# Kernel optimization log

Measured on AMD Instinct MI355X. Metric: run time of the kernel, lower is better.

## Reference

```python
import jax, jax.numpy as jnp
import numpy as np

B, T, F = 8, 4096, 256

def setup_inputs() -> dict:
    key = jax.random.key(0)
    ks = jax.random.split(key, 10)
    s = 1.0 / np.sqrt(F)
    return {
        "x": jax.random.normal(ks[0], (B, T, F), dtype=jnp.float32),
        "Wq_w": jax.random.normal(ks[1], (F, F), dtype=jnp.float32) * s,
        "Wq_b": jax.random.normal(ks[2], (F,), dtype=jnp.float32) * 0.01,
        "Wk_w": jax.random.normal(ks[3], (F, F), dtype=jnp.float32) * s,
        "Wk_b": jax.random.normal(ks[4], (F,), dtype=jnp.float32) * 0.01,
        "Wv_w": jax.random.normal(ks[5], (F, F), dtype=jnp.float32) * s,
        "Wv_b": jax.random.normal(ks[6], (F,), dtype=jnp.float32) * 0.01,
        "w": jax.random.normal(ks[7], (T, T), dtype=jnp.float32) * 0.02,
        "out_w": jax.random.normal(ks[8], (F, F), dtype=jnp.float32) * s,
        "out_b": jax.random.normal(ks[9], (F,), dtype=jnp.float32) * 0.01,
    }

def reference(x, Wq_w, Wq_b, Wk_w, Wk_b, Wv_w, Wv_b, w, out_w, out_b):
    # Linear layers (torch convention: y = x @ W.T + b)
    Q = x @ Wq_w.T + Wq_b                      # [B, T, F]
    K = x @ Wk_w.T + Wk_b                      # [B, T, F]
    V = x @ Wv_w.T + Wv_b                      # [B, T, F]
    Q_sig = jax.nn.sigmoid(Q)
    # Stabilized exponentials (faithful: w over rows, K over FEATURE dim)
    exp_w = jnp.exp(w - jnp.max(w, axis=-1, keepdims=True))        # [T, T]
    exp_K = jnp.exp(K - jnp.max(K, axis=-1, keepdims=True))        # [B, T, F]
    num = jnp.einsum('ts,bsf->btf', exp_w, exp_K * V)              # [B, T, F]
    den = jnp.einsum('ts,bsf->btf', exp_w, exp_K)                  # [B, T, F]
    Yt = Q_sig * (num / den)
    return Yt @ out_w.T + out_b
```

## Files before the change

### kernel.cpp

```cpp
#include <hip/hip_runtime.h>
#include <hip/hip_bf16.h>

#define BB 8
#define TT 4096
#define FF 256
#define BT 32768

typedef unsigned short u16;
typedef __attribute__((ext_vector_type(8))) short short8;
typedef __attribute__((ext_vector_type(4))) float f32x4;
typedef __attribute__((ext_vector_type(4))) unsigned int u32x4;

static __device__ __forceinline__ float bf2f(u16 u) {
    union { unsigned int i; float f; } v; v.i = ((unsigned int)u) << 16; return v.f;
}
static __device__ __forceinline__ u16 f2bf(float f) {
    union { float f; unsigned int i; } v; v.f = f;
    unsigned int x = v.i;
    return (u16)((x + 0x7fffu + ((x >> 16) & 1u)) >> 16);
}

typedef const __attribute__((address_space(1))) void gvoid_t;
typedef __attribute__((address_space(3))) void svoid_t;

__global__ __launch_bounds__(256) void expw_kernel(const float* __restrict__ w,
                                                   u16* __restrict__ ew) {
    __shared__ float red[256];
    int row = blockIdx.x;
    int tid = threadIdx.x;
    const float* wr = w + (size_t)row * TT;

    f32x4 vals[4];
    float m = -1e30f;
#pragma unroll
    for (int v = 0; v < 4; ++v) {
        int idx = (v * 256 + tid) * 4;
        vals[v] = *(const f32x4*)(wr + idx);
#pragma unroll
        for (int j = 0; j < 4; ++j) m = fmaxf(m, vals[v][j]);
    }
    red[tid] = m;
    __syncthreads();
    for (int s = 128; s > 0; s >>= 1) {
        if (tid < s) red[tid] = fmaxf(red[tid], red[tid + s]);
        __syncthreads();
    }
    float rm = red[0];
#pragma unroll
    for (int v = 0; v < 4; ++v) {
        int idx = (v * 256 + tid) * 4;
        float e0 = expf(vals[v][0] - rm), e1 = expf(vals[v][1] - rm);
        float e2 = expf(vals[v][2] - rm), e3 = expf(vals[v][3] - rm);
        uint2 pk;
        pk.x = (unsigned int)f2bf(e0) | ((unsigned int)f2bf(e1) << 16);
        pk.y = (unsigned int)f2bf(e2) | ((unsigned int)f2bf(e3) << 16);
        *(uint2*)(ew + (size_t)row * TT + idx) = pk;
    }
}

__global__ __launch_bounds__(256) void cvt_bf16_kernel(const float* __restrict__ in,
                                                       u16* __restrict__ out, int n4) {
    int i = blockIdx.x * 256 + threadIdx.x;
    if (i < n4) {
        f32x4 v = ((const f32x4*)in)[i];
        uint2 pk;
        pk.x = (unsigned int)f2bf(v[0]) | ((unsigned int)f2bf(v[1]) << 16);
        pk.y = (unsigned int)f2bf(v[2]) | ((unsigned int)f2bf(v[3]) << 16);
        ((uint2*)out)[i] = pk;
    }
}

__global__ __launch_bounds__(256) void cvt_weights_kernel(const float* __restrict__ wq,
                                                          const float* __restrict__ wo,
                                                          const float* __restrict__ wk,
                                                          const float* __restrict__ wv,
                                                          u16* __restrict__ wqb,
                                                          u16* __restrict__ wob,
                                                          u16* __restrict__ wkv) {
    int i = blockIdx.x * 256 + threadIdx.x;
    int which = i >> 14, j = i & 16383;
    int idx = j * 4;
    if (which == 0) {
        f32x4 v = *(const f32x4*)(wq + idx);
        uint2 pk;
        pk.x = (unsigned int)f2bf(v[0]) | ((unsigned int)f2bf(v[1]) << 16);
        pk.y = (unsigned int)f2bf(v[2]) | ((unsigned int)f2bf(v[3]) << 16);
        *(uint2*)(wqb + idx) = pk;
    } else if (which == 1) {
        f32x4 v = *(const f32x4*)(wo + idx);
        uint2 pk;
        pk.x = (unsigned int)f2bf(v[0]) | ((unsigned int)f2bf(v[1]) << 16);
        pk.y = (unsigned int)f2bf(v[2]) | ((unsigned int)f2bf(v[3]) << 16);
        *(uint2*)(wob + idx) = pk;
    } else {
        int f = idx >> 8, c = idx & 255;
        f32x4 a = *(const f32x4*)(wk + idx);
        f32x4 b = *(const f32x4*)(wv + idx);
        uint2 pa, pb;
        pa.x = (unsigned int)f2bf(a[0]) | ((unsigned int)f2bf(a[1]) << 16);
        pa.y = (unsigned int)f2bf(a[2]) | ((unsigned int)f2bf(a[3]) << 16);
        pb.x = (unsigned int)f2bf(b[0]) | ((unsigned int)f2bf(b[1]) << 16);
        pb.y = (unsigned int)f2bf(b[2]) | ((unsigned int)f2bf(b[3]) << 16);
        *(uint2*)(wkv + (size_t)(2 * f) * 256 + c) = pa;
        *(uint2*)(wkv + (size_t)(2 * f + 1) * 256 + c) = pb;
    }
}

template <int MODE>
__global__ __launch_bounds__(256) void gemm_nt(const u16* __restrict__ A,
                                               const u16* __restrict__ Bm,
                                               const float* __restrict__ bias,
                                               void* __restrict__ Call,
                                               int M, int N, int K) {
    __shared__ u16 As[128 * 32];
    __shared__ u16 Bs[128 * 32];

    int tid = threadIdx.x;
    int lane = tid & 63;
    int w = tid >> 6;
    int wr = w >> 1, wc = w & 1;
    int fr = lane & 15, kg = lane >> 4;

    f32x4 acc[4][4];
#pragma unroll
    for (int m = 0; m < 4; ++m)
#pragma unroll
        for (int n = 0; n < 4; ++n) acc[m][n] = (f32x4){0.f, 0.f, 0.f, 0.f};

    int bm = blockIdx.x, bn = blockIdx.y;
    int nk = K >> 5;

    int srow = tid >> 2;
    int schunk = (tid & 3) << 3;
    const u16* aBase = A + (size_t)(bm * 128 + srow) * K + schunk;
    const u16* bBase = Bm + (size_t)(bn * 128 + srow) * K + schunk;
    size_t half = (size_t)64 * K;

    for (int kt = 0; kt < nk; ++kt) {
        __syncthreads();
        int ko = kt << 5;
        __builtin_amdgcn_global_load_lds((gvoid_t*)(aBase + ko), (svoid_t*)&As[tid * 8], 16, 0, 0);
        __builtin_amdgcn_global_load_lds((gvoid_t*)(aBase + half + ko), (svoid_t*)&As[2048 + tid * 8], 16, 0, 0);
        __builtin_amdgcn_global_load_lds((gvoid_t*)(bBase + ko), (svoid_t*)&Bs[tid * 8], 16, 0, 0);
        __builtin_amdgcn_global_load_lds((gvoid_t*)(bBase + half + ko), (svoid_t*)&Bs[2048 + tid * 8], 16, 0, 0);
        __syncthreads();

        short8 af[4], bfr[4];
#pragma unroll
        for (int m = 0; m < 4; ++m)
            af[m] = *(const short8*)&As[(wr * 64 + m * 16 + fr) * 32 + kg * 8];
#pragma unroll
        for (int n = 0; n < 4; ++n)
            bfr[n] = *(const short8*)&Bs[(wc * 64 + n * 16 + fr) * 32 + kg * 8];
#pragma unroll
        for (int m = 0; m < 4; ++m)
#pragma unroll
            for (int n = 0; n < 4; ++n)
                acc[m][n] = __builtin_amdgcn_mfma_f32_16x16x32_bf16(af[m], bfr[n], acc[m][n], 0, 0, 0);
    }

    int row0 = bm * 128 + wr * 64;
    int col0 = bn * 128 + wc * 64;
#pragma unroll
    for (int n = 0; n < 4; ++n) {
        int col = col0 + n * 16 + fr;
        float bv = bias ? bias[col] : 0.0f;
#pragma unroll
        for (int m = 0; m < 4; ++m) {
            int rbase = row0 + m * 16 + kg * 4;
#pragma unroll
            for (int i = 0; i < 4; ++i) {
                float val = acc[m][n][i] + bv;
                size_t idx = (size_t)(rbase + i) * N + col;
                if (MODE == 0)
                    ((float*)Call)[idx] = val;
                else if (MODE == 1)
                    ((u16*)Call)[idx] = f2bf(1.0f / (1.0f + expf(-val)));
                else
                    ((u16*)Call)[idx] = f2bf(val);
            }
        }
    }
}

__global__ __launch_bounds__(512) void kv_mt_kernel(const u16* __restrict__ xbf,
                                                    const u16* __restrict__ wkv,
                                                    const float* __restrict__ bk,
                                                    const float* __restrict__ bv,
                                                    u16* __restrict__ mt) {
    __shared__ u16 As[128 * 32];
    __shared__ u16 Bs[512 * 32];
    __shared__ float rmax4[128][4];

    int tid = threadIdx.x;
    int lane = tid & 63, wid = tid >> 6;
    int fr = lane & 15, kg = lane >> 4;
    int wr = wid >> 2, wc = wid & 3;
    int row0g = blockIdx.x * 128;

    f32x4 acc[4][8];
#pragma unroll
    for (int m = 0; m < 4; ++m)
#pragma unroll
        for (int n = 0; n < 8; ++n) acc[m][n] = (f32x4){0.f, 0.f, 0.f, 0.f};

    const u16* aSrc = xbf + (size_t)(row0g + (tid >> 2)) * 256 + (tid & 3) * 8;
    const u16* bSrc = wkv + (size_t)(tid >> 2) * 256 + (tid & 3) * 8;

    for (int ks = 0; ks < 8; ++ks) {
        __syncthreads();
        __builtin_amdgcn_global_load_lds((gvoid_t*)(aSrc + ks * 32), (svoid_t*)&As[tid * 8], 16, 0, 0);
#pragma unroll
        for (int c = 0; c < 4; ++c)
            __builtin_amdgcn_global_load_lds((gvoid_t*)(bSrc + (size_t)c * 128 * 256 + ks * 32),
                                             (svoid_t*)&Bs[c * 4096 + tid * 8], 16, 0, 0);
        __syncthreads();

        short8 af[4], bfr[8];
#pragma unroll
        for (int m = 0; m < 4; ++m)
            af[m] = *(const short8*)&As[(wr * 64 + m * 16 + fr) * 32 + kg * 8];
#pragma unroll
        for (int n = 0; n < 8; ++n)
            bfr[n] = *(const short8*)&Bs[(wc * 128 + n * 16 + fr) * 32 + kg * 8];
#pragma unroll
        for (int m = 0; m < 4; ++m)
#pragma unroll
            for (int n = 0; n < 8; ++n)
                acc[m][n] = __builtin_amdgcn_mfma_f32_16x16x32_bf16(af[m], bfr[n], acc[m][n], 0, 0, 0);
    }

    int par = fr & 1;
#pragma unroll
    for (int n = 0; n < 8; ++n) {
        int col = wc * 128 + n * 16 + fr;
        int f = col >> 1;
        float bvv = par ? bv[f] : bk[f];
#pragma unroll
        for (int m = 0; m < 4; ++m)
#pragma unroll
            for (int i = 0; i < 4; ++i) acc[m][n][i] += bvv;
    }

    float rmax[4][4];
#pragma unroll
    for (int m = 0; m < 4; ++m)
#pragma unroll
        for (int i = 0; i < 4; ++i) {
            float mx = -1e30f;
#pragma unroll
            for (int n = 0; n < 8; ++n) mx = fmaxf(mx, par ? -1e30f : acc[m][n][i]);
            mx = fmaxf(mx, __shfl_xor(mx, 2));
            mx = fmaxf(mx, __shfl_xor(mx, 4));
            mx = fmaxf(mx, __shfl_xor(mx, 8));
            mx = fmaxf(mx, __shfl_xor(mx, 1));
            rmax[m][i] = mx;
        }
    if (fr == 0) {
#pragma unroll
        for (int m = 0; m < 4; ++m)
#pragma unroll
            for (int i = 0; i < 4; ++i)
                rmax4[wr * 64 + m * 16 + kg * 4 + i][wc] = rmax[m][i];
    }
    __syncthreads();
#pragma unroll
    for (int m = 0; m < 4; ++m)
#pragma unroll
        for (int i = 0; i < 4; ++i) {
            f32x4 r4 = *(const f32x4*)rmax4[wr * 64 + m * 16 + kg * 4 + i];
            rmax[m][i] = fmaxf(fmaxf(r4[0], r4[1]), fmaxf(r4[2], r4[3]));
        }

    int b = row0g >> 12;
    int tcb = (row0g & 4095) + wr * 64;
#pragma unroll
    for (int n = 0; n < 8; ++n) {
        int col = wc * 128 + n * 16 + fr;
        int f = col >> 1;
        size_t rowmt = (size_t)(b * 512 + 2 * f + (par ? 0 : 1));
#pragma unroll
        for (int m = 0; m < 4; ++m) {
            int tc = tcb + m * 16 + kg * 4;
            u16 o[4];
#pragma unroll
            for (int i = 0; i < 4; ++i) {
                float v = acc[m][n][i];
                float ek = expf(v - rmax[m][i]);
                float ekx = __shfl_xor(ek, 1);
                float outv = par ? (ekx * v) : ek;
                o[i] = f2bf(outv);
            }
            uint2 pk;
            pk.x = (unsigned int)o[0] | ((unsigned int)o[1] << 16);
            pk.y = (unsigned int)o[2] | ((unsigned int)o[3] << 16);
            *(uint2*)(mt + rowmt * TT + tc) = pk;
        }
    }
}

#define GLDS(src, eoff) \
    __builtin_amdgcn_global_load_lds((gvoid_t*)(src), (svoid_t*)&L[eoff], 16, 0, 0)

#define STAGE8(P_, KS_) do {                                                   \
    _Pragma("unroll")                                                          \
    for (int i_ = 0; i_ < 4; ++i_) {                                           \
        GLDS(sA + (size_t)i_ * 64 * 4096 + (KS_) * 64,                         \
             (P_) * 16384 + i_ * 4096 + dst);                                  \
        GLDS(sB + (size_t)i_ * 64 * 4096 + (KS_) * 64,                         \
             32768 + (P_) * 16384 + i_ * 4096 + dst);                          \
    }                                                                          \
} while (0)

__global__ __launch_bounds__(512, 2) void gemm256_nt(const u16* __restrict__ A,
                                                     const u16* __restrict__ B,
                                                     const u16* __restrict__ qsig,
                                                     u16* __restrict__ yt) {
    __shared__ u16 L[65536];
    const int K = 4096;
    int tid = threadIdx.x;
    int lane = tid & 63, wid = tid >> 6;
    int fr = lane & 15, kg = lane >> 4;
    int wr = wid >> 2, wc = wid & 3;

    int bid = blockIdx.x;
    int xcd = bid & 7;
    int sl = bid >> 3;
    int bm = (xcd & 3) * 4 + (sl >> 3);
    int bn = (xcd >> 2) * 8 + (sl & 7);

    const char* LB = (const char*)L;

    int x0 = (kg * 16) ^ ((fr & 7) << 4);
    int x1 = (64 + kg * 16) ^ ((fr & 7) << 4);
    int arow = (wr * 128 + fr) * 128;
    int brow = (wc * 64 + fr) * 128;

    int scol = ((tid & 7) * 8) ^ (((tid >> 3) & 7) << 3);
    const u16* sA = A + (size_t)(bm * 256 + (tid >> 3)) * K + scol;
    const u16* sB = B + (size_t)(bn * 256 + (tid >> 3)) * K + scol;
    int dst = tid * 8;

    f32x4 acc[8][4];
#pragma unroll
    for (int m = 0; m < 8; ++m)
#pragma unroll
        for (int n = 0; n < 4; ++n) acc[m][n] = (f32x4){0.f, 0.f, 0.f, 0.f};

    STAGE8(0, 0);
    asm volatile("s_waitcnt vmcnt(0)" ::: "memory");
    __builtin_amdgcn_sched_barrier(0);
    __builtin_amdgcn_s_barrier();

#pragma unroll 1
    for (int t = 0; t < 64; ++t) {
        int p = t & 1;
        const char* abase = LB + p * 32768;
        const char* bbase = LB + 65536 + p * 32768;

        int ks = (t + 1 < 64) ? t + 1 : 0;
        STAGE8(p ^ 1, ks);

        short8 bfr[4][2], af[4][2];
#pragma unroll
        for (int nf = 0; nf < 4; ++nf) {
            const char* rb = bbase + brow + nf * 2048;
            bfr[nf][0] = *(const short8*)(rb + x0);
            bfr[nf][1] = *(const short8*)(rb + x1);
        }
#pragma unroll
        for (int mf = 0; mf < 4; ++mf) {
            const char* rb = abase + arow + mf * 2048;
            af[mf][0] = *(const short8*)(rb + x0);
            af[mf][1] = *(const short8*)(rb + x1);
        }
        asm volatile("s_waitcnt lgkmcnt(0)" ::: "memory");
        __builtin_amdgcn_sched_barrier(0);
        __builtin_amdgcn_s_setprio(1);
#pragma unroll
        for (int mf = 0; mf < 4; ++mf)
#pragma unroll
            for (int nf = 0; nf < 4; ++nf) {
                acc[mf][nf] = __builtin_amdgcn_mfma_f32_16x16x32_bf16(af[mf][0], bfr[nf][0], acc[mf][nf], 0, 0, 0);
                acc[mf][nf] = __builtin_amdgcn_mfma_f32_16x16x32_bf16(af[mf][1], bfr[nf][1], acc[mf][nf], 0, 0, 0);
            }
        __builtin_amdgcn_s_setprio(0);
#pragma unroll
        for (int mf = 0; mf < 4; ++mf) {
            const char* rb = abase + arow + (mf + 4) * 2048;
            af[mf][0] = *(const short8*)(rb + x0);
            af[mf][1] = *(const short8*)(rb + x1);
        }
        asm volatile("s_waitcnt lgkmcnt(0)" ::: "memory");
        __builtin_amdgcn_sched_barrier(0);
        __builtin_amdgcn_s_setprio(1);
#pragma unroll
        for (int mf = 0; mf < 4; ++mf)
#pragma unroll
            for (int nf = 0; nf < 4; ++nf) {
                acc[mf + 4][nf] = __builtin_amdgcn_mfma_f32_16x16x32_bf16(af[mf][0], bfr[nf][0], acc[mf + 4][nf], 0, 0, 0);
                acc[mf + 4][nf] = __builtin_amdgcn_mfma_f32_16x16x32_bf16(af[mf][1], bfr[nf][1], acc[mf + 4][nf], 0, 0, 0);
            }
        __builtin_amdgcn_s_setprio(0);
        asm volatile("s_waitcnt vmcnt(0)" ::: "memory");
        __builtin_amdgcn_sched_barrier(0);
        __builtin_amdgcn_s_barrier();
    }

    int colgb = bn * 256 + wc * 64;
    int row0 = bm * 256 + wr * 128;
    int par = fr & 1;
#pragma unroll
    for (int n = 0; n < 4; ++n) {
        int colg = colgb + n * 16 + fr;
        int b = colg >> 9;
        int f = (colg & 511) >> 1;
#pragma unroll
        for (int m = 0; m < 8; ++m) {
            int tr0 = row0 + m * 16 + kg * 4;
            float v0 = acc[m][n][0], v1 = acc[m][n][1];
            float v2 = acc[m][n][2], v3 = acc[m][n][3];
            float o0 = __shfl_xor(v0, 1), o1 = __shfl_xor(v1, 1);
            float o2 = __shfl_xor(v2, 1), o3 = __shfl_xor(v3, 1);
            float nA = par ? o2 : v0, dA = par ? v2 : o0;
            float nB = par ? o3 : v1, dB = par ? v3 : o1;
            int iA = par ? 2 : 0;
            size_t idxA = ((size_t)(b * 4096 + tr0 + iA) << 8) + f;
            size_t idxB = idxA + 256;
            float qA = bf2f(qsig[idxA]);
            float qB = bf2f(qsig[idxB]);
            yt[idxA] = f2bf(qA * nA * __builtin_amdgcn_rcpf(dA));
            yt[idxB] = f2bf(qB * nB * __builtin_amdgcn_rcpf(dB));
        }
    }
}

extern "C" void kernel_launch(void* const* d_in, const int* in_sizes, int n_in,
                              void* d_out, int out_size, void* d_ws, size_t ws_size,
                              hipStream_t stream) {
    const float* x  = (const float*)d_in[0];
    const float* wq = (const float*)d_in[1];
    const float* bq = (const float*)d_in[2];
    const float* wk = (const float*)d_in[3];
    const float* bk = (const float*)d_in[4];
    const float* wv = (const float*)d_in[5];
    const float* bv = (const float*)d_in[6];
    const float* w  = (const float*)d_in[7];
    const float* wo = (const float*)d_in[8];
    const float* bo = (const float*)d_in[9];

    char* p = (char*)d_ws;
    u16* expw = (u16*)p; p += (size_t)TT * TT * 2;
    u16* xbf  = (u16*)p; p += (size_t)BT * FF * 2;
    u16* wqb  = (u16*)p; p += (size_t)FF * FF * 2;
    u16* wob  = (u16*)p; p += (size_t)FF * FF * 2;
    u16* wkv  = (u16*)p; p += (size_t)2 * FF * FF * 2;
    u16* qsig = (u16*)p; p += (size_t)BT * FF * 2;
    u16* mt   = (u16*)p; p += (size_t)BB * 512 * TT * 2;
    u16* yt = xbf;

    expw_kernel<<<TT, 256, 0, stream>>>(w, expw);

    cvt_bf16_kernel<<<(BT * FF / 4 + 255) / 256, 256, 0, stream>>>(x, xbf, BT * FF / 4);
    cvt_weights_kernel<<<192, 256, 0, stream>>>(wq, wo, wk, wv, wqb, wob, wkv);

    dim3 gp(BT / 128, FF / 128, 1);
    gemm_nt<1><<<gp, 256, 0, stream>>>(xbf, wqb, bq, qsig, BT, FF, FF);

    kv_mt_kernel<<<BT / 128, 512, 0, stream>>>(xbf, wkv, bk, bv, mt);

    gemm256_nt<<<256, 512, 0, stream>>>(expw, mt, qsig, yt);

    gemm_nt<0><<<gp, 256, 0, stream>>>(yt, wob, bo, (float*)d_out, BT, FF, FF);
}
```

Measured before the change: 191.7 us.

## Split GEMM main loop into four phases interleaving staging, LDS reads and MFMA

Splits each k-step of the 256x256 GEMM into four phases, each handling one half of the A or B tile and one k-half of the fragments. Every phase issues a quarter of the next-tile global-to-LDS loads, then its LDS fragment reads, then its MFMAs, with extra workgroup barriers between phases. The aim is to spread memory issue across the compute so loads and MFMA overlap better, and to hold fewer fragment registers (4+4 short8 instead of 8+8). The cost is three more s_barriers per iteration and shorter MFMA bursts, which could leave more time waiting at barriers.

```diff
diff --git a/kernel.cpp b/kernel.cpp
--- a/kernel.cpp
+++ b/kernel.cpp
@@ -302,14 +302,19 @@
 #define GLDS(src, eoff) \
     __builtin_amdgcn_global_load_lds((gvoid_t*)(src), (svoid_t*)&L[eoff], 16, 0, 0)
 
-#define STAGE8(P_, KS_) do {                                                   \
+#define STAGE_H(SRC, RO, P_, H_, KS_) do {                                     \
     _Pragma("unroll")                                                          \
-    for (int i_ = 0; i_ < 4; ++i_) {                                           \
-        GLDS(sA + (size_t)i_ * 64 * 4096 + (KS_) * 64,                         \
-             (P_) * 16384 + i_ * 4096 + dst);                                  \
-        GLDS(sB + (size_t)i_ * 64 * 4096 + (KS_) * 64,                         \
-             32768 + (P_) * 16384 + i_ * 4096 + dst);                          \
+    for (int i2_ = 0; i2_ < 2; ++i2_) {                                        \
+        int i_ = (H_) * 2 + i2_;                                               \
+        GLDS((SRC) + (size_t)i_ * 64 * 4096 + (KS_) * 64,                      \
+             (RO) + (P_) * 16384 + i_ * 4096 + dst);                           \
     }                                                                          \
+} while (0)
+
+#define PH_SYNC() do {                                                         \
+    __builtin_amdgcn_s_barrier();                                              \
+    asm volatile("s_waitcnt lgkmcnt(0)" ::: "memory");                         \
+    __builtin_amdgcn_sched_barrier(0);                                         \
 } while (0)
 
 __global__ __launch_bounds__(512, 2) void gemm256_nt(const u16* __restrict__ A,
@@ -347,7 +352,8 @@
 #pragma unroll
         for (int n = 0; n < 4; ++n) acc[m][n] = (f32x4){0.f, 0.f, 0.f, 0.f};
 
-    STAGE8(0, 0);
+    STAGE_H(sA, 0, 0, 0, 0); STAGE_H(sA, 0, 0, 1, 0);
+    STAGE_H(sB, 32768, 0, 0, 0); STAGE_H(sB, 32768, 0, 1, 0);
     asm volatile("s_waitcnt vmcnt(0)" ::: "memory");
     __builtin_amdgcn_sched_barrier(0);
     __builtin_amdgcn_s_barrier();
@@ -355,52 +361,66 @@
 #pragma unroll 1
     for (int t = 0; t < 64; ++t) {
         int p = t & 1;
+        int q = p ^ 1;
+        int ks = (t + 1 < 64) ? t + 1 : 0;
         const char* abase = LB + p * 32768;
         const char* bbase = LB + 65536 + p * 32768;
 
-        int ks = (t + 1 < 64) ? t + 1 : 0;
-        STAGE8(p ^ 1, ks);
-
-        short8 bfr[4][2], af[4][2];
-#pragma unroll
-        for (int nf = 0; nf < 4; ++nf) {
-            const char* rb = bbase + brow + nf * 2048;
-            bfr[nf][0] = *(const short8*)(rb + x0);
-            bfr[nf][1] = *(const short8*)(rb + x1);
-        }
-#pragma unroll
-        for (int mf = 0; mf < 4; ++mf) {
-            const char* rb = abase + arow + mf * 2048;
-            af[mf][0] = *(const short8*)(rb + x0);
-            af[mf][1] = *(const short8*)(rb + x1);
-        }
-        asm volatile("s_waitcnt lgkmcnt(0)" ::: "memory");
-        __builtin_amdgcn_sched_barrier(0);
+        short8 af[4], bfk[4];
+
+        STAGE_H(sA, 0, q, 0, ks);
+#pragma unroll
+        for (int mf = 0; mf < 4; ++mf) af[mf] = *(const short8*)(abase + arow + mf * 2048 + x0);
+#pragma unroll
+        for (int nf = 0; nf < 4; ++nf) bfk[nf] = *(const short8*)(bbase + brow + nf * 2048 + x0);
+        PH_SYNC();
         __builtin_amdgcn_s_setprio(1);
 #pragma unroll
         for (int mf = 0; mf < 4; ++mf)
 #pragma unroll
-            for (int nf = 0; nf < 4; ++nf) {
-                acc[mf][nf] = __builtin_amdgcn_mfma_f32_16x16x32_bf16(af[mf][0], bfr[nf][0], acc[mf][nf], 0, 0, 0);
-                acc[mf][nf] = __builtin_amdgcn_mfma_f32_16x16x32_bf16(af[mf][1], bfr[nf][1], acc[mf][nf], 0, 0, 0);
-            }
+            for (int nf = 0; nf < 4; ++nf)
+                acc[mf][nf] = __builtin_amdgcn_mfma_f32_16x16x32_bf16(af[mf], bfk[nf], acc[mf][nf], 0, 0, 0);
         __builtin_amdgcn_s_setprio(0);
-#pragma unroll
-        for (int mf = 0; mf < 4; ++mf) {
-            const char* rb = abase + arow + (mf + 4) * 2048;
-            af[mf][0] = *(const short8*)(rb + x0);
-            af[mf][1] = *(const short8*)(rb + x1);
-        }
-        asm volatile("s_waitcnt lgkmcnt(0)" ::: "memory");
-        __builtin_amdgcn_sched_barrier(0);
+        __builtin_amdgcn_s_barrier();
+
+        STAGE_H(sA, 0, q, 1, ks);
+#pragma unroll
+        for (int mf = 0; mf < 4; ++mf) af[mf] = *(const short8*)(abase + arow + (mf + 4) * 2048 + x0);
+        PH_SYNC();
         __builtin_amdgcn_s_setprio(1);
 #pragma unroll
         for (int mf = 0; mf < 4; ++mf)
 #pragma unroll
-            for (int nf = 0; nf < 4; ++nf) {
-                acc[mf + 4][nf] = __builtin_amdgcn_mfma_f32_16x16x32_bf16(af[mf][0], bfr[nf][0], acc[mf + 4][nf], 0, 0, 0);
-                acc[mf + 4][nf] = __builtin_amdgcn_mfma_f32_16x16x32_bf16(af[mf][1], bfr[nf][1], acc[mf + 4][nf], 0, 0, 0);
-            }
+            for (int nf = 0; nf < 4; ++nf)
+                acc[mf + 4][nf] = __builtin_amdgcn_mfma_f32_16x16x32_bf16(af[mf], bfk[nf], acc[mf + 4][nf], 0, 0, 0);
+        __builtin_amdgcn_s_setprio(0);
+        __builtin_amdgcn_s_barrier();
+
+        STAGE_H(sB, 32768, q, 0, ks);
+#pragma unroll
+        for (int mf = 0; mf < 4; ++mf) af[mf] = *(const short8*)(abase + arow + mf * 2048 + x1);
+#pragma unroll
+        for (int nf = 0; nf < 4; ++nf) bfk[nf] = *(const short8*)(bbase + brow + nf * 2048 + x1);
+        PH_SYNC();
+        __builtin_amdgcn_s_setprio(1);
+#pragma unroll
+        for (int mf = 0; mf < 4; ++mf)
+#pragma unroll
+            for (int nf = 0; nf < 4; ++nf)
+                acc[mf][nf] = __builtin_amdgcn_mfma_f32_16x16x32_bf16(af[mf], bfk[nf], acc[mf][nf], 0, 0, 0);
+        __builtin_amdgcn_s_setprio(0);
+        __builtin_amdgcn_s_barrier();
+
+        STAGE_H(sB, 32768, q, 1, ks);
+#pragma unroll
+        for (int mf = 0; mf < 4; ++mf) af[mf] = *(const short8*)(abase + arow + (mf + 4) * 2048 + x1);
+        PH_SYNC();
+        __builtin_amdgcn_s_setprio(1);
+#pragma unroll
+        for (int mf = 0; mf < 4; ++mf)
+#pragma unroll
+            for (int nf = 0; nf < 4; ++nf)
+                acc[mf + 4][nf] = __builtin_amdgcn_mfma_f32_16x16x32_bf16(af[mf], bfk[nf], acc[mf + 4][nf], 0, 0, 0);
         __builtin_amdgcn_s_setprio(0);
         asm volatile("s_waitcnt vmcnt(0)" ::: "memory");
         __builtin_amdgcn_sched_barrier(0);
```

Result: slower. 200.3 us (+4.5%).

## Switch big GEMM to 4-stage ring buffer with 32-wide K steps

Applied to the files above, without the earlier changes.

Restructures the main bf16 GEMM main loop from double-buffered 64-wide K tiles into a four-slot ring of 32-wide K tiles, keeping two tiles of global-to-LDS loads in flight (vmcnt(4)) instead of waiting for all loads each iteration. Fragment reads from LDS are issued before the next prefetch, and the swizzle and staging layout change to match the 64-byte rows. This aims to hide global memory latency better, at the cost of twice as many iterations and barriers per tile.

```diff
diff --git a/kernel.cpp b/kernel.cpp
--- a/kernel.cpp
+++ b/kernel.cpp
@@ -302,14 +302,11 @@
 #define GLDS(src, eoff) \
     __builtin_amdgcn_global_load_lds((gvoid_t*)(src), (svoid_t*)&L[eoff], 16, 0, 0)
 
-#define STAGE8(P_, KS_) do {                                                   \
-    _Pragma("unroll")                                                          \
-    for (int i_ = 0; i_ < 4; ++i_) {                                           \
-        GLDS(sA + (size_t)i_ * 64 * 4096 + (KS_) * 64,                         \
-             (P_) * 16384 + i_ * 4096 + dst);                                  \
-        GLDS(sB + (size_t)i_ * 64 * 4096 + (KS_) * 64,                         \
-             32768 + (P_) * 16384 + i_ * 4096 + dst);                          \
-    }                                                                          \
+#define STAGE4(Q_, KS_) do {                                                   \
+    GLDS(sA + (KS_) * 32, (Q_) * 8192 + dst);                                  \
+    GLDS(sA + (size_t)128 * 4096 + (KS_) * 32, (Q_) * 8192 + 4096 + dst);      \
+    GLDS(sB + (KS_) * 32, 32768 + (Q_) * 8192 + dst);                          \
+    GLDS(sB + (size_t)128 * 4096 + (KS_) * 32, 32768 + (Q_) * 8192 + 4096 + dst); \
 } while (0)
 
 __global__ __launch_bounds__(512, 2) void gemm256_nt(const u16* __restrict__ A,
@@ -331,14 +328,13 @@
 
     const char* LB = (const char*)L;
 
-    int x0 = (kg * 16) ^ ((fr & 7) << 4);
-    int x1 = (64 + kg * 16) ^ ((fr & 7) << 4);
-    int arow = (wr * 128 + fr) * 128;
-    int brow = (wc * 64 + fr) * 128;
-
-    int scol = ((tid & 7) * 8) ^ (((tid >> 3) & 7) << 3);
-    const u16* sA = A + (size_t)(bm * 256 + (tid >> 3)) * K + scol;
-    const u16* sB = B + (size_t)(bn * 256 + (tid >> 3)) * K + scol;
+    int xsw = (kg * 16) ^ (((fr >> 1) & 3) << 4);
+    int arow = (wr * 128 + fr) * 64;
+    int brow = (wc * 64 + fr) * 64;
+
+    int scol = ((tid & 3) ^ ((tid >> 3) & 3)) * 8;
+    const u16* sA = A + (size_t)(bm * 256 + (tid >> 2)) * K + scol;
+    const u16* sB = B + (size_t)(bn * 256 + (tid >> 2)) * K + scol;
     int dst = tid * 8;
 
     f32x4 acc[8][4];
@@ -347,62 +343,41 @@
 #pragma unroll
         for (int n = 0; n < 4; ++n) acc[m][n] = (f32x4){0.f, 0.f, 0.f, 0.f};
 
-    STAGE8(0, 0);
-    asm volatile("s_waitcnt vmcnt(0)" ::: "memory");
+    STAGE4(0, 0);
+    STAGE4(1, 1);
+    asm volatile("s_waitcnt vmcnt(4)" ::: "memory");
     __builtin_amdgcn_sched_barrier(0);
     __builtin_amdgcn_s_barrier();
 
 #pragma unroll 1
-    for (int t = 0; t < 64; ++t) {
-        int p = t & 1;
-        const char* abase = LB + p * 32768;
-        const char* bbase = LB + 65536 + p * 32768;
-
-        int ks = (t + 1 < 64) ? t + 1 : 0;
-        STAGE8(p ^ 1, ks);
-
-        short8 bfr[4][2], af[4][2];
-#pragma unroll
-        for (int nf = 0; nf < 4; ++nf) {
-            const char* rb = bbase + brow + nf * 2048;
-            bfr[nf][0] = *(const short8*)(rb + x0);
-            bfr[nf][1] = *(const short8*)(rb + x1);
-        }
-#pragma unroll
-        for (int mf = 0; mf < 4; ++mf) {
-            const char* rb = abase + arow + mf * 2048;
-            af[mf][0] = *(const short8*)(rb + x0);
-            af[mf][1] = *(const short8*)(rb + x1);
-        }
+    for (int t = 0; t < 128; ++t) {
+        int p = t & 3;
+        int q = (t + 2) & 3;
+        int ks = (t + 2 < 128) ? t + 2 : 0;
+        const char* abase = LB + p * 16384;
+        const char* bbase = LB + 65536 + p * 16384;
+
+        short8 af[8], bfr[4];
+#pragma unroll
+        for (int nf = 0; nf < 4; ++nf)
+            bfr[nf] = *(const short8*)(bbase + brow + nf * 1024 + xsw);
+#pragma unroll
+        for (int mf = 0; mf < 8; ++mf)
+            af[mf] = *(const short8*)(abase + arow + mf * 1024 + xsw);
+
+        STAGE4(q, ks);
+
         asm volatile("s_waitcnt lgkmcnt(0)" ::: "memory");
         __builtin_amdgcn_sched_barrier(0);
         __builtin_amdgcn_s_setprio(1);
 #pragma unroll
-        for (int mf = 0; mf < 4; ++mf)
-#pragma unroll
-            for (int nf = 0; nf < 4; ++nf) {
-                acc[mf][nf] = __builtin_amdgcn_mfma_f32_16x16x32_bf16(af[mf][0], bfr[nf][0], acc[mf][nf], 0, 0, 0);
-                acc[mf][nf] = __builtin_amdgcn_mfma_f32_16x16x32_bf16(af[mf][1], bfr[nf][1], acc[mf][nf], 0, 0, 0);
-            }
+        for (int mf = 0; mf < 8; ++mf)
+#pragma unroll
+            for (int nf = 0; nf < 4; ++nf)
+                acc[mf][nf] = __builtin_amdgcn_mfma_f32_16x16x32_bf16(af[mf], bfr[nf], acc[mf][nf], 0, 0, 0);
         __builtin_amdgcn_s_setprio(0);
-#pragma unroll
-        for (int mf = 0; mf < 4; ++mf) {
-            const char* rb = abase + arow + (mf + 4) * 2048;
-            af[mf][0] = *(const short8*)(rb + x0);
-            af[mf][1] = *(const short8*)(rb + x1);
-        }
-        asm volatile("s_waitcnt lgkmcnt(0)" ::: "memory");
-        __builtin_amdgcn_sched_barrier(0);
-        __builtin_amdgcn_s_setprio(1);
-#pragma unroll
-        for (int mf = 0; mf < 4; ++mf)
-#pragma unroll
-            for (int nf = 0; nf < 4; ++nf) {
-                acc[mf + 4][nf] = __builtin_amdgcn_mfma_f32_16x16x32_bf16(af[mf][0], bfr[nf][0], acc[mf + 4][nf], 0, 0, 0);
-                acc[mf + 4][nf] = __builtin_amdgcn_mfma_f32_16x16x32_bf16(af[mf][1], bfr[nf][1], acc[mf + 4][nf], 0, 0, 0);
-            }
-        __builtin_amdgcn_s_setprio(0);
-        asm volatile("s_waitcnt vmcnt(0)" ::: "memory");
+
+        asm volatile("s_waitcnt vmcnt(4)" ::: "memory");
         __builtin_amdgcn_sched_barrier(0);
         __builtin_amdgcn_s_barrier();
     }
```

New measurement: 190.1 us. About the same (-0.8%).
